# Kernel tuning notes

Measured on AMD Instinct MI355X. Metric: run time of the kernel, lower is better.

The kernel has to match this reference:

```python
import jax, jax.numpy as jnp
import numpy as np

B, T, TB, TV, TR = 4, 512, 512, 512, 256
D, H = 1024, 16
HD = D // H
D4 = D // 4
DFF = 4096
ROPE_THETA = 10000.0


def _rms(x, w, eps=1e-6):
    return x * jax.lax.rsqrt(jnp.mean(x * x, -1, keepdims=True) + eps) * w


def _ln(x, w, b, eps=1e-5):
    m = jnp.mean(x, -1, keepdims=True)
    v = jnp.var(x, -1, keepdims=True)
    return (x - m) * jax.lax.rsqrt(v + eps) * w + b


def _rope_cs(L, hd):
    inv = 1.0 / (ROPE_THETA ** (jnp.arange(0, hd, 2, dtype=jnp.float32) / hd))
    f = jnp.arange(L, dtype=jnp.float32)[:, None] * inv[None, :]
    e = jnp.concatenate([f, f], -1)  # (L, hd)
    return jnp.cos(e), jnp.sin(e)


def _rot_half(x):
    h = x.shape[-1] // 2
    return jnp.concatenate([-x[..., h:], x[..., :h]], -1)


def _rope(x, cos, sin):
    return x * cos + _rot_half(x) * sin


def _heads(x):
    b, l, _ = x.shape
    return x.reshape(b, l, H, HD).transpose(0, 2, 1, 3)  # (B,H,L,hd)


def setup_inputs() -> dict:
    key = jax.random.key(0)
    ks = jax.random.split(key, 16)
    def n(k, shape, s=0.02):
        return jax.random.normal(k, shape, jnp.float32) * s
    return {
        'x': n(ks[0], (B, T, D), 1.0),
        'bev_tokens': n(ks[1], (B, TB, D), 1.0),
        'vl_tokens': n(ks[2], (B, TV, D), 1.0),
        'reasoning_tokens': n(ks[3], (B, TR, D), 1.0),
        'conditioning': n(ks[4], (B, D), 1.0),
        'ln_pre_w': jnp.ones((D,)), 'ln_pre_b': jnp.zeros((D,)),
        'adaln_w': n(ks[5], (6 * D, D)), 'adaln_b': jnp.zeros((6 * D,)),
        'q_proj_w': n(ks[6], (D, D)), 'q_proj_b': jnp.zeros((D,)),
        'qa_w': n(ks[7], (3, D4, D)), 'qa_b': jnp.zeros((3, D4)),
        'qa_out_w': n(ks[8], (D, D4)), 'qa_out_b': jnp.zeros((D,)),
        'k_w': n(ks[9], (4, D, D)), 'k_b': jnp.zeros((4, D)),
        'v_w': n(ks[10], (4, D, D)), 'v_b': jnp.zeros((4, D)),
        'o_w': n(ks[11], (D, D)), 'o_b': jnp.zeros((D,)),
        'qn_w': jnp.ones((HD,)), 'kn_w': jnp.ones((HD,)),
        'gating': jnp.full((1,), 0.5, jnp.float32),
        'temps': jnp.zeros((4,)), 'score_biases': jnp.zeros((4,)),
        'ffn_ln_w': jnp.ones((D,)), 'ffn_ln_b': jnp.zeros((D,)),
        'ffn_w1': n(ks[12], (DFF, D)), 'ffn_b1': jnp.zeros((DFF,)),
        'ffn_w2': n(ks[13], (D, DFF)), 'ffn_b2': jnp.zeros((D,)),
    }


def reference(x, bev_tokens, vl_tokens, reasoning_tokens, conditioning,
              ln_pre_w, ln_pre_b, adaln_w, adaln_b,
              q_proj_w, q_proj_b, qa_w, qa_b, qa_out_w, qa_out_b,
              k_w, k_b, v_w, v_b, o_w, o_b, qn_w, kn_w,
              gating, temps, score_biases,
              ffn_ln_w, ffn_ln_b, ffn_w1, ffn_b1, ffn_w2, ffn_b2):
    # AdaLN modulation (T_route == 0 path: single modulation for whole sequence)
    mod = jax.nn.silu(conditioning) @ adaln_w.T + adaln_b  # (B, 6D)
    shift_pre, scale_pre, gate_attn, shift_ffn, scale_ffn, gate_ffn = jnp.split(mod, 6, axis=1)
    x_norm = _ln(x, ln_pre_w, ln_pre_b) * (1.0 + scale_pre[:, None, :]) + shift_pre[:, None, :]

    # Self Q and per-source K/V (sources: self, bev, vl, reasoning)
    q_self = _heads(x_norm @ q_proj_w.T + q_proj_b)
    srcs = [x_norm, bev_tokens, vl_tokens, reasoning_tokens]
    k_all = [_heads(s @ k_w[i].T + k_b[i]) for i, s in enumerate(srcs)]
    v_all = [_heads(s @ v_w[i].T + v_b[i]) for i, s in enumerate(srcs)]

    # Source-specific adapter queries: d -> d/4 -> d (shared out proj)
    q_ad = [_heads((x_norm @ qa_w[i].T + qa_b[i]) @ qa_out_w.T + qa_out_b) for i in range(3)]

    # QK-Norm (RMSNorm on head_dim)
    q_all = [_rms(q, qn_w) for q in [q_self] + q_ad]
    k_all = [_rms(k, kn_w) for k in k_all]

    # RoPE: Q and K for self-attention; K only for cross sources
    cosT, sinT = _rope_cs(x.shape[1], HD)
    q_all[0] = _rope(q_all[0], cosT, sinT)
    k_roped = []
    for k in k_all:
        c, s = _rope_cs(k.shape[2], HD)
        k_roped.append(_rope(k, c, s))

    # Per-source temperature / bias; gating only on reasoning scores
    temp = 1.0 + jax.nn.softplus(temps)
    ratio_g = jnp.tanh(gating[0])
    inv_sqrt_d = HD ** -0.5
    scores = []
    for i in range(4):
        s = jnp.einsum('bhqd,bhkd->bhqk', q_all[i], k_roped[i]) * (inv_sqrt_d * temp[i]) + score_biases[i]
        if i == 3:
            s = s * ratio_g
        scores.append(s)

    attn = jax.nn.softmax(jnp.concatenate(scores, -1), axis=-1)  # joint softmax
    v_cat = jnp.concatenate(v_all, 2)  # (B,H,T+TB+TV+TR,hd)
    out = jnp.einsum('bhqk,bhkd->bhqd', attn, v_cat)
    out = out.transpose(0, 2, 1, 3).reshape(x.shape) @ o_w.T + o_b
    x = x + gate_attn[:, None, :] * out

    # FFN with AdaLN modulation (dropout = identity at eval)
    h = _ln(x, ffn_ln_w, ffn_ln_b) * (1.0 + scale_ffn[:, None, :]) + shift_ffn[:, None, :]
    h = jax.nn.gelu(h @ ffn_w1.T + ffn_b1, approximate=False) @ ffn_w2.T + ffn_b2
    return x + gate_ffn[:, None, :] * h
```

## Files before the change

### kernel.cpp

```cpp
#include <hip/hip_runtime.h>

typedef unsigned short ushort_t;
typedef __attribute__((ext_vector_type(8))) __bf16 bf16x8;
typedef __attribute__((ext_vector_type(4))) float f32x4;

__device__ __forceinline__ float bf2f(ushort_t u) {
    union { unsigned int i; float f; } v; v.i = ((unsigned int)u) << 16; return v.f;
}
__device__ __forceinline__ ushort_t f2bf(float f) {
    union { float f; unsigned int i; } v; v.f = f;
    unsigned int r = (v.i + 0x7FFFu + ((v.i >> 16) & 1u)) >> 16;
    return (ushort_t)r;
}
__device__ __forceinline__ float gelu_exact(float v) {
    return 0.5f * v * (1.f + erff(v * 0.70710678118654752f));
}
__device__ __forceinline__ float ld1(const void* p, size_t i, int isf32) {
    return isf32 ? ((const float*)p)[i] : bf2f(((const ushort_t*)p)[i]);
}
__device__ __forceinline__ void stage8(const void* p, size_t idx, int isf32, ushort_t* dst) {
    if (isf32) {
        const float* f = (const float*)p + idx;
        float4 u = *(const float4*)f;
        float4 v = *(const float4*)(f + 4);
        dst[0] = f2bf(u.x); dst[1] = f2bf(u.y); dst[2] = f2bf(u.z); dst[3] = f2bf(u.w);
        dst[4] = f2bf(v.x); dst[5] = f2bf(v.y); dst[6] = f2bf(v.z); dst[7] = f2bf(v.w);
    } else {
        *(uint4*)dst = *(const uint4*)((const ushort_t*)p + idx);
    }
}
__device__ __forceinline__ void gload16(const ushort_t* g, ushort_t* l) {
    __builtin_amdgcn_global_load_lds(
        (const __attribute__((address_space(1))) unsigned int*)g,
        (__attribute__((address_space(3))) unsigned int*)l, 16, 0, 0);
}

__device__ __forceinline__ void store_q(ushort_t* qbuf, int row, int c, int p0, float v) {
    int b = row >> 9, t = row & 511;
    qbuf[((((size_t)(b * 16 + (c >> 6))) * 4 + p0) * 512 + t) * 64 + (c & 63)] = f2bf(v);
}
__device__ __forceinline__ void store_k(ushort_t* kbuf, int row, int c, int koff, int p1, float v) {
    int b = row >> p1, t = row & ((1 << p1) - 1);
    kbuf[(((size_t)(b * 16 + (c >> 6))) * 1792 + koff + t) * 64 + (c & 63)] = f2bf(v);
}
__device__ __forceinline__ void store_v(ushort_t* vbufT, int row, int c, int koff, int p1, float v) {
    int b = row >> p1, t = row & ((1 << p1) - 1);
    vbufT[(((size_t)(b * 16 + (c >> 6))) * 64 + (c & 63)) * 1792 + koff + t] = f2bf(v);
}

__global__ void detect_kernel(const unsigned int* __restrict__ x, int* __restrict__ flag) {
    if (threadIdx.x == 0 && blockIdx.x == 0) {
        int sane = 0;
        for (int i = 0; i < 256; i++) {
            unsigned int e = (x[i] >> 7) & 0xFFu;
            if (e == 0u || (e >= 100u && e <= 140u)) sane++;
        }
        *flag = (sane >= 200) ? 0 : 1;
    }
}

__global__ void prep_rope_kernel(float* __restrict__ tab) {
    int idx = blockIdx.x * 256 + threadIdx.x;
    int t = idx >> 5, d = idx & 31;
    float ang = (float)t * __expf(-(float)d * (9.210340371976184f / 32.f));
    float cs, sn;
    sincosf(ang, &sn, &cs);
    tab[idx * 2]     = cs;
    tab[idx * 2 + 1] = sn;
}

static constexpr size_t CW_QPROJ = 0;
static constexpr size_t CW_QA    = 1048576;
static constexpr size_t CW_QAOUT = 1835008;
static constexpr size_t CW_KW    = 2097152;
static constexpr size_t CW_VW    = 6291456;
static constexpr size_t CW_OW    = 10485760;
static constexpr size_t CW_FFN1  = 11534336;
static constexpr size_t CW_FFN2  = 15728640;
static constexpr size_t CW_TOTAL = 19922944;

__global__ void __launch_bounds__(256) convert_weights_kernel(
    const void* s0, const void* s1, const void* s2, const void* s3,
    const void* s4, const void* s5, const void* s6, const void* s7,
    ushort_t* __restrict__ dst, const int* __restrict__ dflag) {
    int isf32 = *dflag;
    size_t i8 = ((size_t)blockIdx.x * 256 + threadIdx.x) * 8;
    if (i8 >= CW_TOTAL) return;
    const void* src; size_t base;
    if      (i8 < CW_QA)    { src = s0; base = CW_QPROJ; }
    else if (i8 < CW_QAOUT) { src = s1; base = CW_QA; }
    else if (i8 < CW_KW)    { src = s2; base = CW_QAOUT; }
    else if (i8 < CW_VW)    { src = s3; base = CW_KW; }
    else if (i8 < CW_OW)    { src = s4; base = CW_VW; }
    else if (i8 < CW_FFN1)  { src = s5; base = CW_OW; }
    else if (i8 < CW_FFN2)  { src = s6; base = CW_FFN1; }
    else                    { src = s7; base = CW_FFN2; }
    ushort_t t8[8];
    stage8(src, i8 - base, isf32, t8);
    *(uint4*)(dst + i8) = *(uint4*)t8;
}

__global__ void __launch_bounds__(256) convert_act3_kernel(
    const void* __restrict__ bev, const void* __restrict__ vl,
    const void* __restrict__ reas, ushort_t* __restrict__ actA,
    ushort_t* __restrict__ actB, const int* __restrict__ dflag) {
    int isf32 = *dflag;
    size_t i8 = ((size_t)blockIdx.x * 256 + threadIdx.x) * 8;
    if (i8 >= 5242880) return;
    ushort_t t8[8];
    if (i8 < 2097152) {
        stage8(bev, i8, isf32, t8);
        *(uint4*)(actA + i8) = *(uint4*)t8;
    } else if (i8 < 4194304) {
        stage8(vl, i8 - 2097152, isf32, t8);
        *(uint4*)(actA + i8) = *(uint4*)t8;
    } else {
        stage8(reas, i8 - 4194304, isf32, t8);
        *(uint4*)(actB + (i8 - 4194304)) = *(uint4*)t8;
    }
}

__global__ void prep_consts_kernel(const void* __restrict__ temps,
                                   const void* __restrict__ biases,
                                   const void* __restrict__ gating,
                                   float* __restrict__ consts,
                                   const int* __restrict__ dflag) {
    if (threadIdx.x == 0 && blockIdx.x == 0) {
        int isf32 = *dflag;
        float g = tanhf(ld1(gating, 0, isf32));
        for (int s = 0; s < 4; s++) {
            float t  = ld1(temps, s, isf32);
            float sp = (t > 20.f) ? t : log1pf(expf(t));
            float scale = 0.125f * (1.f + sp);
            float mul = (s == 3) ? g : 1.f;
            consts[s]     = scale * mul;
            consts[4 + s] = ld1(biases, s, isf32) * mul;
        }
    }
}

__global__ void __launch_bounds__(256) adaln_kernel(
    const void* __restrict__ cond, const void* __restrict__ w,
    const void* __restrict__ bias, float* __restrict__ mod,
    int wmode, const int* __restrict__ dflag) {
    __shared__ float cs[1024];
    int isf32 = *dflag;
    int wf = (wmode == 2) ? 0 : isf32;
    int b = blockIdx.y, tid = threadIdx.x;
    for (int i = tid; i < 1024; i += 256) {
        float c = ld1(cond, b * 1024 + i, isf32);
        cs[i] = c / (1.f + expf(-c));
    }
    __syncthreads();
    int n = blockIdx.x * 256 + tid;
    float acc = 0.f;
    if (wf) {
        const float* wr = (const float*)w + (size_t)n * 1024;
        for (int d = 0; d < 1024; d += 8) {
            float4 a = *(const float4*)(wr + d);
            float4 bb = *(const float4*)(wr + d + 4);
            acc += cs[d+0]*a.x + cs[d+1]*a.y + cs[d+2]*a.z + cs[d+3]*a.w
                 + cs[d+4]*bb.x + cs[d+5]*bb.y + cs[d+6]*bb.z + cs[d+7]*bb.w;
        }
    } else {
        const ushort_t* wr = (const ushort_t*)w + (size_t)n * 1024;
        for (int d = 0; d < 1024; d += 8) {
            uint4 raw = *(const uint4*)(wr + d);
            const ushort_t* u = (const ushort_t*)&raw;
            acc += cs[d+0]*bf2f(u[0]) + cs[d+1]*bf2f(u[1]) + cs[d+2]*bf2f(u[2]) + cs[d+3]*bf2f(u[3])
                 + cs[d+4]*bf2f(u[4]) + cs[d+5]*bf2f(u[5]) + cs[d+6]*bf2f(u[6]) + cs[d+7]*bf2f(u[7]);
        }
    }
    mod[(size_t)b * 6144 + n] = acc + ld1(bias, n, isf32);
}

template <int SRC>
__global__ void __launch_bounds__(256) ln_mod_kernel(
    const void* __restrict__ xin, const float* __restrict__ mod,
    const void* __restrict__ lnw, const void* __restrict__ lnb,
    int shift_off, int scale_off, ushort_t* __restrict__ out,
    const int* __restrict__ dflag) {
    int isf32 = *dflag;
    int row = blockIdx.x, tid = threadIdx.x;
    int b = row >> 9;
    float v[4];
    #pragma unroll
    for (int i = 0; i < 4; i++) {
        size_t idx = (size_t)row * 1024 + tid + 256 * i;
        v[i] = (SRC == 1) ? ((const float*)xin)[idx] : ld1(xin, idx, isf32);
    }
    float s = v[0] + v[1] + v[2] + v[3];
    float ss = v[0]*v[0] + v[1]*v[1] + v[2]*v[2] + v[3]*v[3];
    #pragma unroll
    for (int off = 1; off < 64; off <<= 1) {
        s  += __shfl_xor(s,  off, 64);
        ss += __shfl_xor(ss, off, 64);
    }
    __shared__ float red[8];
    int w = tid >> 6;
    if ((tid & 63) == 0) { red[w] = s; red[4 + w] = ss; }
    __syncthreads();
    s  = red[0] + red[1] + red[2] + red[3];
    ss = red[4] + red[5] + red[6] + red[7];
    float mean = s * (1.f / 1024.f);
    float var  = ss * (1.f / 1024.f) - mean * mean;
    float inv  = rsqrtf(var + 1e-5f);
    const float* mb = mod + (size_t)b * 6144;
    #pragma unroll
    for (int i = 0; i < 4; i++) {
        int d = tid + 256 * i;
        float xn = (v[i] - mean) * inv;
        float y  = xn * ld1(lnw, d, isf32) + ld1(lnb, d, isf32);
        out[(size_t)row * 1024 + d] = f2bf(y * (1.f + mb[scale_off + d]) + mb[shift_off + d]);
    }
}

template <int EPI>
__global__ void __launch_bounds__(256) gemm_bt_kernel(
    const void* __restrict__ A, int lda,
    const void* __restrict__ W, int wrow0,
    const void* __restrict__ bias,
    void* __restrict__ Cout, int ldc, int K, int p0, int p1,
    int a_ext, int wmode, const int* __restrict__ dflag) {
    __shared__ ushort_t As[64][40];
    __shared__ ushort_t Bs[64][40];
    int isf32 = *dflag;
    int fa = a_ext ? isf32 : 0;
    int fw = (wmode == 2) ? 0 : isf32;
    int m0 = blockIdx.x * 64, n0 = blockIdx.y * 64;
    int tid = threadIdx.x;
    int r = tid >> 2, c = (tid & 3) * 8;
    int w = tid >> 6, ln = tid & 63;
    int msub = (w & 1) * 32, nsub = (w >> 1) * 32;
    int fr = ln & 15, q = ln >> 4;
    f32x4 acc00 = {0.f,0.f,0.f,0.f}, acc01 = {0.f,0.f,0.f,0.f};
    f32x4 acc10 = {0.f,0.f,0.f,0.f}, acc11 = {0.f,0.f,0.f,0.f};
    for (int k0 = 0; k0 < K; k0 += 32) {
        __syncthreads();
        {
            ushort_t t8[8];
            stage8(A, (size_t)(m0 + r) * lda + c + k0, fa, t8);
            *(uint4*)&As[r][c] = *(uint4*)t8;
        }
        {
            ushort_t t8[8];
            stage8(W, (size_t)(wrow0 + n0 + r) * K + c + k0, fw, t8);
            *(uint4*)&Bs[r][c] = *(uint4*)t8;
        }
        __syncthreads();
        bf16x8 a0 = *(const bf16x8*)&As[msub + fr][q * 8];
        bf16x8 a1 = *(const bf16x8*)&As[msub + 16 + fr][q * 8];
        bf16x8 b0 = *(const bf16x8*)&Bs[nsub + fr][q * 8];
        bf16x8 b1 = *(const bf16x8*)&Bs[nsub + 16 + fr][q * 8];
        acc00 = __builtin_amdgcn_mfma_f32_16x16x32_bf16(a0, b0, acc00, 0, 0, 0);
        acc01 = __builtin_amdgcn_mfma_f32_16x16x32_bf16(a0, b1, acc01, 0, 0, 0);
        acc10 = __builtin_amdgcn_mfma_f32_16x16x32_bf16(a1, b0, acc10, 0, 0, 0);
        acc11 = __builtin_amdgcn_mfma_f32_16x16x32_bf16(a1, b1, acc11, 0, 0, 0);
    }
    int col0 = n0 + nsub + fr;
    float bv0 = ld1(bias, wrow0 + col0, isf32);
    float bv1 = ld1(bias, wrow0 + col0 + 16, isf32);
    #pragma unroll
    for (int mi = 0; mi < 2; mi++) {
        #pragma unroll
        for (int ni = 0; ni < 2; ni++) {
            f32x4 a = (mi == 0) ? (ni == 0 ? acc00 : acc01) : (ni == 0 ? acc10 : acc11);
            int col = col0 + ni * 16;
            float bb = (ni == 0) ? bv0 : bv1;
            #pragma unroll
            for (int e = 0; e < 4; e++) {
                int rowg = m0 + msub + mi * 16 + q * 4 + e;
                float v = a[e] + bb;
                if (EPI == 2) v = gelu_exact(v);
                if (EPI == 0) {
                    ((float*)Cout)[(size_t)rowg * ldc + col] = v;
                } else if (EPI == 1 || EPI == 2) {
                    ((ushort_t*)Cout)[(size_t)rowg * ldc + col] = f2bf(v);
                } else if (EPI == 3) {
                    store_k((ushort_t*)Cout, rowg, col, p0, p1, v);
                } else if (EPI == 5) {
                    store_v((ushort_t*)Cout, rowg, col, p0, p1, v);
                } else {
                    store_q((ushort_t*)Cout, rowg, col, p0, v);
                }
            }
        }
    }
}

__device__ __forceinline__ void gemm_mainloop(
    const ushort_t* __restrict__ A, int lda,
    const ushort_t* __restrict__ W, int ldw,
    int m0, int wrow0, int kbeg, int klen,
    ushort_t* As, ushort_t* Bs, f32x4 acc[4][4])
{
    const int tid = threadIdx.x;
    const int w = tid >> 6;
    const int ln = tid & 63;
    const int fr = ln & 15, q = ln >> 4;
    const int wm = w & 1, wn = w >> 1;
    const ushort_t* gA = A + (size_t)(m0 + (tid >> 2)) * lda + kbeg + (tid & 3) * 8;
    const ushort_t* gW = W + (size_t)(wrow0 + (tid >> 2)) * ldw + kbeg + (tid & 3) * 8;
    const size_t sA = (size_t)64 * lda;
    const size_t sW = (size_t)64 * ldw;
    ushort_t* lA = As + w * 512;
    ushort_t* lB = Bs + w * 512;
    for (int k = 0; k < klen; k += 32) {
        __syncthreads();
        gload16(gA, lA);
        gload16(gA + sA, lA + 2048);
        gload16(gW, lB);
        gload16(gW + sW, lB + 2048);
        gA += 32; gW += 32;
        __syncthreads();
        bf16x8 af[4], bfr[4];
        #pragma unroll
        for (int mi = 0; mi < 4; mi++)
            af[mi] = *(const bf16x8*)&As[(wm * 64 + mi * 16 + fr) * 32 + q * 8];
        #pragma unroll
        for (int ni = 0; ni < 4; ni++)
            bfr[ni] = *(const bf16x8*)&Bs[(wn * 64 + ni * 16 + fr) * 32 + q * 8];
        #pragma unroll
        for (int mi = 0; mi < 4; mi++)
            #pragma unroll
            for (int ni = 0; ni < 4; ni++)
                acc[mi][ni] = __builtin_amdgcn_mfma_f32_16x16x32_bf16(af[mi], bfr[ni], acc[mi][ni], 0, 0, 0);
    }
}

__global__ void __launch_bounds__(256) gemm_stage1_kernel(
    const ushort_t* __restrict__ xnorm,
    const ushort_t* __restrict__ actA, const ushort_t* __restrict__ actB,
    const ushort_t* __restrict__ Wq, const ushort_t* __restrict__ Wqa,
    const ushort_t* __restrict__ Wk, const ushort_t* __restrict__ Wv,
    const void* __restrict__ bq, const void* __restrict__ bqa,
    const void* __restrict__ bk, const void* __restrict__ bv,
    const void* __restrict__ qnw, const void* __restrict__ knw,
    const float* __restrict__ ropetab,
    ushort_t* __restrict__ qbuf, ushort_t* __restrict__ qah,
    ushort_t* __restrict__ kbuf, ushort_t* __restrict__ vbufT,
    const int* __restrict__ dflag)
{
    __shared__ ushort_t As[4096], Bs[4096];
    int isf32 = *dflag;
    int bid = blockIdx.x;
    int mode, koff = 0, p1 = 9, srow0, wrow0, am0, boff = 0;
    const ushort_t* A;
    const ushort_t* W;
    const void* bias;
    if (bid < 480) {
        int bx = bid % 16, by = bid / 16;
        am0 = bx * 128; srow0 = am0;
        int n0 = by * 128;
        A = xnorm;
        if (n0 < 1024)      { mode = 0; W = Wq;  bias = bq;  wrow0 = n0; }
        else if (n0 < 1792) { mode = 1; W = Wqa; bias = bqa; wrow0 = n0 - 1024; }
        else if (n0 < 2816) { mode = 2; W = Wk;  bias = bk;  wrow0 = n0 - 1792; }
        else                { mode = 3; W = Wv;  bias = bv;  wrow0 = n0 - 2816; }
    } else {
        int id2 = bid - 480;
        int mb = id2 % 40, ny = id2 / 40;
        int src;
        if (mb < 16)      { src = 0; A = actA; am0 = mb * 128;        srow0 = am0;             koff = 512;  p1 = 9; }
        else if (mb < 32) { src = 1; A = actA; am0 = mb * 128;        srow0 = (mb - 16) * 128; koff = 1024; p1 = 9; }
        else              { src = 2; A = actB; am0 = (mb - 32) * 128; srow0 = am0;             koff = 1536; p1 = 8; }
        int n0 = ny * 128;
        int isK = (n0 < 1024);
        wrow0 = isK ? n0 : n0 - 1024;
        W = (isK ? Wk : Wv) + (size_t)(src + 1) * 1048576;
        bias = isK ? bk : bv;
        boff = (src + 1) * 1024;
        mode = isK ? 2 : 3;
    }
    f32x4 acc[4][4];
    #pragma unroll
    for (int i = 0; i < 4; i++)
        #pragma unroll
        for (int j = 0; j < 4; j++) acc[i][j] = (f32x4){0.f, 0.f, 0.f, 0.f};
    gemm_mainloop(A, 1024, W, 1024, am0, wrow0, 0, 1024, As, Bs, acc);
    int tid = threadIdx.x, w = tid >> 6, ln = tid & 63;
    int fr = ln & 15, q = tid & 63; q = (ln >> 4);
    int wm = w & 1, wn = w >> 1;
    float bb[4], nw[4];
    #pragma unroll
    for (int ni = 0; ni < 4; ni++)
        bb[ni] = ld1(bias, boff + wrow0 + wn * 64 + ni * 16 + fr, isf32);
    if (mode == 0 || mode == 2) {
        const void* nwp = (mode == 0) ? qnw : knw;
        #pragma unroll
        for (int ni = 0; ni < 4; ni++) nw[ni] = ld1(nwp, ni * 16 + fr, isf32);
    }
    const int tmask = (1 << p1) - 1;
    #pragma unroll
    for (int mi = 0; mi < 4; mi++) {
        #pragma unroll
        for (int e = 0; e < 4; e++) {
            int row = srow0 + wm * 64 + mi * 16 + q * 4 + e;
            float v0 = acc[mi][0][e] + bb[0];
            float v1 = acc[mi][1][e] + bb[1];
            float v2 = acc[mi][2][e] + bb[2];
            float v3 = acc[mi][3][e] + bb[3];
            int c0 = wrow0 + wn * 64 + fr;
            if (mode == 1) {
                qah[(size_t)row * 768 + c0]      = f2bf(v0);
                qah[(size_t)row * 768 + c0 + 16] = f2bf(v1);
                qah[(size_t)row * 768 + c0 + 32] = f2bf(v2);
                qah[(size_t)row * 768 + c0 + 48] = f2bf(v3);
            } else if (mode == 3) {
                store_v(vbufT, row, c0,      koff, p1, v0);
                store_v(vbufT, row, c0 + 16, koff, p1, v1);
                store_v(vbufT, row, c0 + 32, koff, p1, v2);
                store_v(vbufT, row, c0 + 48, koff, p1, v3);
            } else {
                float ss = v0*v0 + v1*v1 + v2*v2 + v3*v3;
                ss += __shfl_xor(ss, 1, 64);
                ss += __shfl_xor(ss, 2, 64);
                ss += __shfl_xor(ss, 4, 64);
                ss += __shfl_xor(ss, 8, 64);
                float inv = rsqrtf(ss * (1.f / 64.f) + 1e-6f);
                float y0 = v0 * inv * nw[0];
                float y1 = v1 * inv * nw[1];
                float y2 = v2 * inv * nw[2];
                float y3 = v3 * inv * nw[3];
                int t = row & tmask;
                float2 cs0 = *(const float2*)&ropetab[((t << 5) + fr) * 2];
                float2 cs1 = *(const float2*)&ropetab[((t << 5) + 16 + fr) * 2];
                float r0 = y0 * cs0.x - y2 * cs0.y;
                float r1 = y1 * cs1.x - y3 * cs1.y;
                float r2 = y2 * cs0.x + y0 * cs0.y;
                float r3 = y3 * cs1.x + y1 * cs1.y;
                if (mode == 0) {
                    store_q(qbuf, row, c0,      0, r0);
                    store_q(qbuf, row, c0 + 16, 0, r1);
                    store_q(qbuf, row, c0 + 32, 0, r2);
                    store_q(qbuf, row, c0 + 48, 0, r3);
                } else {
                    store_k(kbuf, row, c0,      koff, p1, r0);
                    store_k(kbuf, row, c0 + 16, koff, p1, r1);
                    store_k(kbuf, row, c0 + 32, koff, p1, r2);
                    store_k(kbuf, row, c0 + 48, koff, p1, r3);
                }
            }
        }
    }
}

__global__ void __launch_bounds__(256) gemm_qaout_kernel(
    const ushort_t* __restrict__ qah,
    const ushort_t* __restrict__ W, const void* __restrict__ bias,
    const void* __restrict__ qnw,
    ushort_t* __restrict__ qbuf, const int* __restrict__ dflag)
{
    __shared__ ushort_t As[4096], Bs[4096];
    int isf32 = *dflag;
    int m0 = blockIdx.x * 128, n0 = blockIdx.y * 128;
    int z = blockIdx.z;
    const ushort_t* A = qah + (size_t)z * 256;
    f32x4 acc[4][4];
    #pragma unroll
    for (int i = 0; i < 4; i++)
        #pragma unroll
        for (int j = 0; j < 4; j++) acc[i][j] = (f32x4){0.f, 0.f, 0.f, 0.f};
    gemm_mainloop(A, 768, W, 256, m0, n0, 0, 256, As, Bs, acc);
    int tid = threadIdx.x, w = tid >> 6, ln = tid & 63;
    int fr = ln & 15, q = ln >> 4, wm = w & 1, wn = w >> 1;
    float bb[4], nw[4];
    #pragma unroll
    for (int ni = 0; ni < 4; ni++) {
        bb[ni] = ld1(bias, n0 + wn * 64 + ni * 16 + fr, isf32);
        nw[ni] = ld1(qnw, ni * 16 + fr, isf32);
    }
    #pragma unroll
    for (int mi = 0; mi < 4; mi++) {
        #pragma unroll
        for (int e = 0; e < 4; e++) {
            int row = m0 + wm * 64 + mi * 16 + q * 4 + e;
            float v0 = acc[mi][0][e] + bb[0];
            float v1 = acc[mi][1][e] + bb[1];
            float v2 = acc[mi][2][e] + bb[2];
            float v3 = acc[mi][3][e] + bb[3];
            float ss = v0*v0 + v1*v1 + v2*v2 + v3*v3;
            ss += __shfl_xor(ss, 1, 64);
            ss += __shfl_xor(ss, 2, 64);
            ss += __shfl_xor(ss, 4, 64);
            ss += __shfl_xor(ss, 8, 64);
            float inv = rsqrtf(ss * (1.f / 64.f) + 1e-6f);
            int c0 = n0 + wn * 64 + fr;
            store_q(qbuf, row, c0,      1 + z, v0 * inv * nw[0]);
            store_q(qbuf, row, c0 + 16, 1 + z, v1 * inv * nw[1]);
            store_q(qbuf, row, c0 + 32, 1 + z, v2 * inv * nw[2]);
            store_q(qbuf, row, c0 + 48, 1 + z, v3 * inv * nw[3]);
        }
    }
}

template <int EPI>
__global__ void __launch_bounds__(256) gemm_plain_kernel(
    const ushort_t* __restrict__ A, int lda,
    const ushort_t* __restrict__ W, int ldw,
    const void* __restrict__ bias,
    void* __restrict__ o0, void* __restrict__ o1,
    void* __restrict__ o2, void* __restrict__ o3,
    int ldc, int ksub, const int* __restrict__ dflag)
{
    __shared__ ushort_t As[4096], Bs[4096];
    int isf32 = *dflag;
    int m0 = blockIdx.x * 128, n0 = blockIdx.y * 128;
    int z = blockIdx.z;
    void* Cout = (z == 0) ? o0 : (z == 1) ? o1 : (z == 2) ? o2 : o3;
    f32x4 acc[4][4];
    #pragma unroll
    for (int i = 0; i < 4; i++)
        #pragma unroll
        for (int j = 0; j < 4; j++) acc[i][j] = (f32x4){0.f, 0.f, 0.f, 0.f};
    gemm_mainloop(A, lda, W, ldw, m0, n0, z * ksub, ksub, As, Bs, acc);
    int tid = threadIdx.x, w = tid >> 6, ln = tid & 63;
    int fr = ln & 15, q = ln >> 4, wm = w & 1, wn = w >> 1;
    #pragma unroll
    for (int ni = 0; ni < 4; ni++) {
        int c = n0 + wn * 64 + ni * 16 + fr;
        float bb = (z == 0) ? ld1(bias, c, isf32) : 0.f;
        #pragma unroll
        for (int mi = 0; mi < 4; mi++) {
            #pragma unroll
            for (int e = 0; e < 4; e++) {
                int row = m0 + wm * 64 + mi * 16 + q * 4 + e;
                float v = acc[mi][ni][e] + bb;
                if (EPI == 2) {
                    ((ushort_t*)Cout)[(size_t)row * ldc + c] = f2bf(gelu_exact(v));
                } else {
                    ((float*)Cout)[(size_t)row * ldc + c] = v;
                }
            }
        }
    }
}

__global__ void __launch_bounds__(256) qrope_ip_kernel(
    ushort_t* __restrict__ qbuf, const void* __restrict__ qnw,
    const int* __restrict__ dflag) {
    int isf32 = *dflag;
    int w = threadIdx.x >> 6, ln = threadIdx.x & 63;
    int flat = blockIdx.x * 4 + w;
    int t = flat & 511, s = (flat >> 9) & 3;
    ushort_t* p = qbuf + (size_t)flat * 64;
    float x = bf2f(p[ln]);
    float ssum = x * x;
    #pragma unroll
    for (int off = 1; off < 64; off <<= 1) ssum += __shfl_xor(ssum, off, 64);
    float y = x * rsqrtf(ssum * (1.f / 64.f) + 1e-6f) * ld1(qnw, ln, isf32);
    if (s == 0) {
        float ang = (float)t * __expf(-(float)(ln & 31) * (9.210340371976184f / 32.f));
        float cs, sn;
        sincosf(ang, &sn, &cs);
        float other = __shfl_xor(y, 32, 64);
        y = y * cs + ((ln < 32) ? -other : other) * sn;
    }
    p[ln] = f2bf(y);
}

__global__ void __launch_bounds__(256) krope_ip_kernel(
    ushort_t* __restrict__ kbuf, const void* __restrict__ knw,
    const int* __restrict__ dflag) {
    int isf32 = *dflag;
    int w = threadIdx.x >> 6, ln = threadIdx.x & 63;
    int flat = blockIdx.x * 4 + w;
    int j = flat % 1792;
    int t = j & 511;
    ushort_t* p = kbuf + (size_t)flat * 64;
    float x = bf2f(p[ln]);
    float ssum = x * x;
    #pragma unroll
    for (int off = 1; off < 64; off <<= 1) ssum += __shfl_xor(ssum, off, 64);
    float y = x * rsqrtf(ssum * (1.f / 64.f) + 1e-6f) * ld1(knw, ln, isf32);
    float ang = (float)t * __expf(-(float)(ln & 31) * (9.210340371976184f / 32.f));
    float cs, sn;
    sincosf(ang, &sn, &cs);
    float other = __shfl_xor(y, 32, 64);
    y = y * cs + ((ln < 32) ? -other : other) * sn;
    p[ln] = f2bf(y);
}

__global__ void __launch_bounds__(256) attn_mfma_kernel(
    const ushort_t* __restrict__ qbuf, const ushort_t* __restrict__ kbuf,
    const ushort_t* __restrict__ vbufT, const float* __restrict__ consts,
    float* __restrict__ pacc0, float* __restrict__ pacc1,
    float* __restrict__ pml) {
    __shared__ ushort_t ks[64][72];
    __shared__ ushort_t vsT[64][72];
    __shared__ ushort_t ps[4][16][72];
    int id = blockIdx.x;
    int g  = (id & 7) | ((id >> 6) << 3);
    int qx = (id >> 3) & 7;
    int bh = g & 63;
    int z  = g >> 6;
    int tid = threadIdx.x, w = tid >> 6, ln = tid & 63;
    int r0 = qx * 64 + w * 16;
    int m = ln & 15, quad = ln >> 4;
    const int ntile = z ? 12 : 16;
    const int keybase = z * 1024;
    const int s0i = z * 2;

    const ushort_t* qb = qbuf + (size_t)bh * 4 * 512 * 64;
    bf16x8 qA0f = *(const bf16x8*)(qb + ((size_t)(s0i * 512 + r0 + m)) * 64 + quad * 8);
    bf16x8 qA1f = *(const bf16x8*)(qb + ((size_t)(s0i * 512 + r0 + m)) * 64 + 32 + quad * 8);
    bf16x8 qB0f = *(const bf16x8*)(qb + ((size_t)((s0i + 1) * 512 + r0 + m)) * 64 + quad * 8);
    bf16x8 qB1f = *(const bf16x8*)(qb + ((size_t)((s0i + 1) * 512 + r0 + m)) * 64 + 32 + quad * 8);

    const float aA = consts[s0i],     bA = consts[4 + s0i];
    const float aB = consts[s0i + 1], bB = consts[4 + s0i + 1];

    float m_i[4], l_i[4];
    f32x4 acc[4];
    #pragma unroll
    for (int e = 0; e < 4; e++) { m_i[e] = -1e30f; l_i[e] = 0.f; }
    #pragma unroll
    for (int d = 0; d < 4; d++) acc[d] = (f32x4){0.f, 0.f, 0.f, 0.f};

    const ushort_t* kb  = kbuf  + (size_t)bh * 1792 * 64 + (size_t)keybase * 64;
    const ushort_t* vbT = vbufT + (size_t)bh * 64 * 1792 + keybase;
    int skey = tid >> 3, sd = (tid & 7) * 8;
    uint4 kreg0 = *(const uint4*)(kb + (size_t)skey * 64 + sd);
    uint4 kreg1 = *(const uint4*)(kb + (size_t)(skey + 32) * 64 + sd);
    uint4 vreg0 = *(const uint4*)(vbT + (size_t)skey * 1792 + sd);
    uint4 vreg1 = *(const uint4*)(vbT + (size_t)(skey + 32) * 1792 + sd);
    *(uint4*)&ks[skey][sd]       = kreg0;
    *(uint4*)&ks[skey + 32][sd]  = kreg1;
    *(uint4*)&vsT[skey][sd]      = vreg0;
    *(uint4*)&vsT[skey + 32][sd] = vreg1;
    __syncthreads();

    for (int ti = 0; ti < ntile; ti++) {
        const bool pf = (ti + 1 < ntile);
        if (pf) {
            int nx = (ti + 1) * 64;
            kreg0 = *(const uint4*)(kb + (size_t)(nx + skey) * 64 + sd);
            kreg1 = *(const uint4*)(kb + (size_t)(nx + skey + 32) * 64 + sd);
            vreg0 = *(const uint4*)(vbT + (size_t)skey * 1792 + nx + sd);
            vreg1 = *(const uint4*)(vbT + (size_t)(skey + 32) * 1792 + nx + sd);
        }
        int sl = (ti >= 8) ? 1 : 0;
        float a_s = sl ? aB : aA;
        float b_s = sl ? bB : bA;
        bf16x8 qA0 = sl ? qB0f : qA0f;
        bf16x8 qA1 = sl ? qB1f : qA1f;
        f32x4 zero = {0.f, 0.f, 0.f, 0.f};
        bf16x8 k0a = *(const bf16x8*)&ks[m][quad * 8];
        bf16x8 k0b = *(const bf16x8*)&ks[m][32 + quad * 8];
        bf16x8 k1a = *(const bf16x8*)&ks[16 + m][quad * 8];
        bf16x8 k1b = *(const bf16x8*)&ks[16 + m][32 + quad * 8];
        bf16x8 k2a = *(const bf16x8*)&ks[32 + m][quad * 8];
        bf16x8 k2b = *(const bf16x8*)&ks[32 + m][32 + quad * 8];
        bf16x8 k3a = *(const bf16x8*)&ks[48 + m][quad * 8];
        bf16x8 k3b = *(const bf16x8*)&ks[48 + m][32 + quad * 8];
        f32x4 sc0 = __builtin_amdgcn_mfma_f32_16x16x32_bf16(qA0, k0a, zero, 0, 0, 0);
        sc0 = __builtin_amdgcn_mfma_f32_16x16x32_bf16(qA1, k0b, sc0, 0, 0, 0);
        f32x4 sc1 = __builtin_amdgcn_mfma_f32_16x16x32_bf16(qA0, k1a, zero, 0, 0, 0);
        sc1 = __builtin_amdgcn_mfma_f32_16x16x32_bf16(qA1, k1b, sc1, 0, 0, 0);
// ... 183 lines not shown
            bf16x8 pA0 = *(const bf16x8*)&ps[w][m][quad * 8];
            bf16x8 pA1 = *(const bf16x8*)&ps[w][m][32 + quad * 8];
            #pragma unroll
            for (int dsub = 0; dsub < 4; dsub++) {
                bf16x8 vB0 = *(const bf16x8*)&vsT[p][dsub * 16 + m][quad * 8];
                bf16x8 vB1 = *(const bf16x8*)&vsT[p][dsub * 16 + m][32 + quad * 8];
                acc[dsub] = __builtin_amdgcn_mfma_f32_16x16x32_bf16(pA0, vB0, acc[dsub], 0, 0, 0);
                acc[dsub] = __builtin_amdgcn_mfma_f32_16x16x32_bf16(pA1, vB1, acc[dsub], 0, 0, 0);
            }
            if (tcnt < 27) {
                *(uint4*)&ks[1 - p][skey][sd]       = kreg0;
                *(uint4*)&ks[1 - p][skey + 32][sd]  = kreg1;
                *(uint4*)&vsT[1 - p][skey][sd]      = vreg0;
                *(uint4*)&vsT[1 - p][skey + 32][sd] = vreg1;
            }
            __syncthreads();
            p ^= 1;
            tcnt++;
        }
    }
    #pragma unroll
    for (int e = 0; e < 4; e++) {
        float l = l_i[e];
        #pragma unroll
        for (int off = 1; off < 16; off <<= 1) l += __shfl_xor(l, off, 64);
        float invl = 1.f / l;
        int t = r0 + quad * 4 + e;
        #pragma unroll
        for (int dsub = 0; dsub < 4; dsub++) {
            int d = dsub * 16 + m;
            attn_out[(((size_t)(b * 512 + t)) * 16 + h) * 64 + d] = f2bf(acc[dsub][e] * invl);
        }
    }
}

__global__ void resgate_kernel(const void* __restrict__ x, const float* __restrict__ p0,
                               const float* __restrict__ p1, const float* __restrict__ p2,
                               const float* __restrict__ p3,
                               const float* __restrict__ mod, float* __restrict__ x1,
                               int sum4, const int* __restrict__ dflag) {
    int isf32 = *dflag;
    int i = blockIdx.x * 256 + threadIdx.x;
    int b = i >> 19, n = i & 1023;
    float proj = p0[i];
    if (sum4) proj += p1[i] + p2[i] + p3[i];
    x1[i] = ld1(x, i, isf32) + mod[(size_t)b * 6144 + 2048 + n] * proj;
}
__global__ void final_kernel(const float* __restrict__ x1, const float* __restrict__ f0,
                             const float* __restrict__ f1, const float* __restrict__ f2,
                             const float* __restrict__ f3,
                             const float* __restrict__ mod, void* __restrict__ out,
                             int sum4, const int* __restrict__ dflag) {
    int isf32 = *dflag;
    int i = blockIdx.x * 256 + threadIdx.x;
    int b = i >> 19, n = i & 1023;
    float ffn = f0[i];
    if (sum4) ffn += f1[i] + f2[i] + f3[i];
    float val = x1[i] + mod[(size_t)b * 6144 + 5120 + n] * ffn;
    if (isf32) ((float*)out)[i] = val;
    else       ((ushort_t*)out)[i] = f2bf(val);
}

static constexpr size_t OFF_CONSTS   = 0;
static constexpr size_t OFF_FLAG     = 64;
static constexpr size_t OFF_MOD      = 512;
static constexpr size_t OFF_XNORM    = OFF_MOD    + 98304;
static constexpr size_t OFF_QAH      = OFF_XNORM  + 4194304;
static constexpr size_t OFF_KBUF     = OFF_XNORM  + 8388608;
static constexpr size_t OFF_VBUF     = OFF_KBUF   + 14680064;
static constexpr size_t OFF_QBUF     = OFF_VBUF   + 14680064;
static constexpr size_t OFF_ATTNOUT  = OFF_QBUF   + 16777216;
static constexpr size_t OFF_WCACHE   = OFF_ATTNOUT + 4194304;
static constexpr size_t OFF_PACC1    = OFF_WCACHE + CW_TOTAL * 2;
static constexpr size_t OFF_PML      = OFF_PACC1  + 8388608;
static constexpr size_t OFF_ROPE     = OFF_PML    + 524288;
static constexpr size_t WS_NEED      = OFF_WCACHE + 52428800;

extern "C" void kernel_launch(void* const* d_in, const int* in_sizes, int n_in,
                              void* d_out, int out_size, void* d_ws, size_t ws_size,
                              hipStream_t stream) {
    (void)in_sizes; (void)n_in; (void)out_size;
    const void* x        = d_in[0];
    const void* bev      = d_in[1];
    const void* vl       = d_in[2];
    const void* reas     = d_in[3];
    const void* cond     = d_in[4];
    const void* ln_pre_w = d_in[5];
    const void* ln_pre_b = d_in[6];
    const void* adaln_w  = d_in[7];
    const void* adaln_b  = d_in[8];
    const void* q_proj_w = d_in[9];
    const void* q_proj_b = d_in[10];
    const void* qa_w     = d_in[11];
    const void* qa_b     = d_in[12];
    const void* qa_out_w = d_in[13];
    const void* qa_out_b = d_in[14];
    const void* k_w      = d_in[15];
    const void* k_b      = d_in[16];
    const void* v_w      = d_in[17];
    const void* v_b      = d_in[18];
    const void* o_w      = d_in[19];
    const void* o_b      = d_in[20];
    const void* qn_w     = d_in[21];
    const void* kn_w     = d_in[22];
    const void* gating   = d_in[23];
    const void* temps    = d_in[24];
    const void* sbias    = d_in[25];
    const void* ffn_ln_w = d_in[26];
    const void* ffn_ln_b = d_in[27];
    const void* ffn_w1   = d_in[28];
    const void* ffn_b1   = d_in[29];
    const void* ffn_w2   = d_in[30];
    const void* ffn_b2   = d_in[31];

    char* ws = (char*)d_ws;
    float*    consts   = (float*)(ws + OFF_CONSTS);
    int*      dflag    = (int*)(ws + OFF_FLAG);
    float*    mod      = (float*)(ws + OFF_MOD);
    ushort_t* xnorm    = (ushort_t*)(ws + OFF_XNORM);
    ushort_t* qah      = (ushort_t*)(ws + OFF_QAH);
    ushort_t* kbuf     = (ushort_t*)(ws + OFF_KBUF);
    ushort_t* vbufT    = (ushort_t*)(ws + OFF_VBUF);
    ushort_t* qbuf     = (ushort_t*)(ws + OFF_QBUF);
    ushort_t* attnout  = (ushort_t*)(ws + OFF_ATTNOUT);
    float*    x1       = (float*)(ws + OFF_XNORM);
    ushort_t* hmid     = (ushort_t*)(ws + OFF_KBUF);
    ushort_t* hin      = (ushort_t*)(ws + OFF_ATTNOUT);
    ushort_t* wc       = (ushort_t*)(ws + OFF_WCACHE);
    float*    ropetab  = (float*)(ws + OFF_ROPE);
    float*    pacc0    = (float*)(ws + OFF_XNORM);
    float*    pacc1    = (float*)(ws + OFF_PACC1);
    float*    pml      = (float*)(ws + OFF_PML);
    ushort_t* actA     = (ushort_t*)(ws + OFF_PACC1);
    ushort_t* actB     = (ushort_t*)(ws + OFF_ATTNOUT);
    float*    op0      = (float*)(ws + OFF_KBUF);
    float*    op1      = (float*)(ws + OFF_KBUF + 8388608);
    float*    op2      = (float*)(ws + OFF_KBUF + 16777216);
    float*    op3      = (float*)(ws + OFF_QBUF);
    float*    f0       = (float*)(ws + OFF_QBUF);
    float*    f1       = (float*)(ws + OFF_QBUF + 8388608);
    float*    f2       = (float*)(ws + OFF_KBUF + 16777216);
    float*    f3       = (float*)(ws + OFF_PACC1);

    const bool use_cache = (ws_size >= WS_NEED);

    detect_kernel<<<1, 64, 0, stream>>>((const unsigned int*)x, dflag);
    prep_consts_kernel<<<1, 64, 0, stream>>>(temps, sbias, gating, consts, dflag);

    if (use_cache) {
        prep_rope_kernel<<<64, 256, 0, stream>>>(ropetab);
        convert_weights_kernel<<<9728, 256, 0, stream>>>(
            q_proj_w, qa_w, qa_out_w, k_w, v_w, o_w, ffn_w1, ffn_w2, wc, dflag);
        convert_act3_kernel<<<2560, 256, 0, stream>>>(bev, vl, reas, actA, actB, dflag);
        adaln_kernel<<<dim3(24, 4), 256, 0, stream>>>(cond, adaln_w, adaln_b, mod, 0, dflag);
        ln_mod_kernel<0><<<2048, 256, 0, stream>>>(x, mod, ln_pre_w, ln_pre_b, 0, 1024, xnorm, dflag);

        gemm_stage1_kernel<<<1120, 256, 0, stream>>>(
            xnorm, actA, actB,
            wc + CW_QPROJ, wc + CW_QA, wc + CW_KW, wc + CW_VW,
            q_proj_b, qa_b, k_b, v_b, qn_w, kn_w, ropetab,
            qbuf, qah, kbuf, vbufT, dflag);
        gemm_qaout_kernel<<<dim3(16, 8, 3), 256, 0, stream>>>(
            qah, wc + CW_QAOUT, qa_out_b, qn_w, qbuf, dflag);

        attn_mfma_kernel<<<1024, 256, 0, stream>>>(
            qbuf, kbuf, vbufT, consts, pacc0, pacc1, pml);
        attn_combine_kernel<<<8192, 256, 0, stream>>>(pacc0, pacc1, pml, attnout);

        gemm_plain_kernel<0><<<dim3(16, 8, 4), 256, 0, stream>>>(
            attnout, 1024, wc + CW_OW, 1024, o_b, op0, op1, op2, op3, 1024, 256, dflag);
        resgate_kernel<<<8192, 256, 0, stream>>>(x, op0, op1, op2, op3, mod, x1, 1, dflag);
        ln_mod_kernel<1><<<2048, 256, 0, stream>>>(x1, mod, ffn_ln_w, ffn_ln_b, 3072, 4096, hin, dflag);
        gemm_plain_kernel<2><<<dim3(16, 32, 1), 256, 0, stream>>>(
            hin, 1024, wc + CW_FFN1, 1024, ffn_b1, hmid, nullptr, nullptr, nullptr, 4096, 1024, dflag);
        gemm_plain_kernel<0><<<dim3(16, 8, 4), 256, 0, stream>>>(
            hmid, 4096, wc + CW_FFN2, 4096, ffn_b2, f0, f1, f2, f3, 1024, 1024, dflag);
        final_kernel<<<8192, 256, 0, stream>>>(x1, f0, f1, f2, f3, mod, d_out, 1, dflag);
    } else {
        float* proj0L = (float*)(ws + OFF_QBUF);
        adaln_kernel<<<dim3(24, 4), 256, 0, stream>>>(cond, adaln_w, adaln_b, mod, 0, dflag);
        ln_mod_kernel<0><<<2048, 256, 0, stream>>>(x, mod, ln_pre_w, ln_pre_b, 0, 1024, xnorm, dflag);
        gemm_bt_kernel<4><<<dim3(32, 16), 256, 0, stream>>>(xnorm, 1024, q_proj_w, 0, q_proj_b, qbuf, 0, 1024, 0, 9, 0, 0, dflag);
        {
            const void* srcs[4] = {xnorm, bev, vl, reas};
            const int koffs[4] = {0, 512, 1024, 1536};
            const int p1s[4]   = {9, 9, 9, 8};
            for (int i = 0; i < 4; i++) {
                int aext = (i == 0) ? 0 : 1;
                int gx = (i == 3) ? 16 : 32;
                gemm_bt_kernel<3><<<dim3(gx, 16), 256, 0, stream>>>(
                    srcs[i], 1024, k_w, i * 1024, k_b, kbuf, 0, 1024, koffs[i], p1s[i], aext, 0, dflag);
                gemm_bt_kernel<5><<<dim3(gx, 16), 256, 0, stream>>>(
                    srcs[i], 1024, v_w, i * 1024, v_b, vbufT, 0, 1024, koffs[i], p1s[i], aext, 0, dflag);
            }
        }
        gemm_bt_kernel<1><<<dim3(32, 12), 256, 0, stream>>>(xnorm, 1024, qa_w, 0, qa_b, qah, 768, 1024, 0, 0, 0, 0, dflag);
        for (int i = 0; i < 3; i++)
            gemm_bt_kernel<4><<<dim3(32, 16), 256, 0, stream>>>(qah + i * 256, 768, qa_out_w, 0, qa_out_b,
                                                                qbuf, 0, 256, 1 + i, 9, 0, 0, dflag);
        qrope_ip_kernel<<<32768, 256, 0, stream>>>(qbuf, qn_w, dflag);
        krope_ip_kernel<<<28672, 256, 0, stream>>>(kbuf, kn_w, dflag);
        attn_mfma_legacy_kernel<<<dim3(8, 64), 256, 0, stream>>>(qbuf, kbuf, vbufT, consts, attnout);
        gemm_bt_kernel<0><<<dim3(32, 16), 256, 0, stream>>>(attnout, 1024, o_w, 0, o_b, proj0L, 1024, 1024, 0, 0, 0, 0, dflag);
        resgate_kernel<<<8192, 256, 0, stream>>>(x, proj0L, proj0L, proj0L, proj0L, mod, x1, 0, dflag);
        ln_mod_kernel<1><<<2048, 256, 0, stream>>>(x1, mod, ffn_ln_w, ffn_ln_b, 3072, 4096, hin, dflag);
        gemm_bt_kernel<2><<<dim3(32, 64), 256, 0, stream>>>(hin, 1024, ffn_w1, 0, ffn_b1, hmid, 4096, 1024, 0, 0, 0, 0, dflag);
        gemm_bt_kernel<0><<<dim3(32, 16), 256, 0, stream>>>(hmid, 4096, ffn_w2, 0, ffn_b2, proj0L, 1024, 4096, 0, 0, 0, 0, dflag);
        final_kernel<<<8192, 256, 0, stream>>>(x1, proj0L, proj0L, proj0L, proj0L, mod, d_out, 0, dflag);
    }
}
```

Measured before the change: 526.3 us.

## Double GEMM K-step, split AdaLN over K with atomics, fuse resgate with LN

```diff
diff --git a/kernel.cpp b/kernel.cpp
--- a/kernel.cpp
+++ b/kernel.cpp
@@ -139,39 +139,46 @@
     }
 }
 
+__global__ void adaln_init_kernel(const void* __restrict__ bias, float* __restrict__ mod,
+                                  const int* __restrict__ dflag) {
+    int isf32 = *dflag;
+    int n = blockIdx.x * 256 + threadIdx.x;
+    float b = ld1(bias, n, isf32);
+    #pragma unroll
+    for (int bb = 0; bb < 4; bb++) mod[(size_t)bb * 6144 + n] = b;
+}
+
 __global__ void __launch_bounds__(256) adaln_kernel(
     const void* __restrict__ cond, const void* __restrict__ w,
-    const void* __restrict__ bias, float* __restrict__ mod,
-    int wmode, const int* __restrict__ dflag) {
-    __shared__ float cs[1024];
-    int isf32 = *dflag;
-    int wf = (wmode == 2) ? 0 : isf32;
-    int b = blockIdx.y, tid = threadIdx.x;
-    for (int i = tid; i < 1024; i += 256) {
-        float c = ld1(cond, b * 1024 + i, isf32);
-        cs[i] = c / (1.f + expf(-c));
+    float* __restrict__ mod, const int* __restrict__ dflag) {
+    __shared__ float cs[256];
+    int isf32 = *dflag;
+    int b = blockIdx.y, z = blockIdx.z, tid = threadIdx.x;
+    {
+        float c = ld1(cond, b * 1024 + z * 256 + tid, isf32);
+        cs[tid] = c / (1.f + expf(-c));
     }
     __syncthreads();
     int n = blockIdx.x * 256 + tid;
     float acc = 0.f;
-    if (wf) {
-        const float* wr = (const float*)w + (size_t)n * 1024;
-        for (int d = 0; d < 1024; d += 8) {
+    if (isf32) {
+        const float* wr = (const float*)w + (size_t)n * 1024 + z * 256;
+        for (int d = 0; d < 256; d += 8) {
             float4 a = *(const float4*)(wr + d);
             float4 bb = *(const float4*)(wr + d + 4);
             acc += cs[d+0]*a.x + cs[d+1]*a.y + cs[d+2]*a.z + cs[d+3]*a.w
                  + cs[d+4]*bb.x + cs[d+5]*bb.y + cs[d+6]*bb.z + cs[d+7]*bb.w;
         }
     } else {
-        const ushort_t* wr = (const ushort_t*)w + (size_t)n * 1024;
-        for (int d = 0; d < 1024; d += 8) {
+        const ushort_t* wr = (const ushort_t*)w + (size_t)n * 1024 + z * 256;
+        for (int d = 0; d < 256; d += 8) {
             uint4 raw = *(const uint4*)(wr + d);
             const ushort_t* u = (const ushort_t*)&raw;
             acc += cs[d+0]*bf2f(u[0]) + cs[d+1]*bf2f(u[1]) + cs[d+2]*bf2f(u[2]) + cs[d+3]*bf2f(u[3])
                  + cs[d+4]*bf2f(u[4]) + cs[d+5]*bf2f(u[5]) + cs[d+6]*bf2f(u[6]) + cs[d+7]*bf2f(u[7]);
         }
     }
-    mod[(size_t)b * 6144 + n] = acc + ld1(bias, n, isf32);
+    atomicAdd(&mod[(size_t)b * 6144 + n], acc);
 }
 
 template <int SRC>
@@ -212,6 +219,51 @@
         float xn = (v[i] - mean) * inv;
         float y  = xn * ld1(lnw, d, isf32) + ld1(lnb, d, isf32);
         out[(size_t)row * 1024 + d] = f2bf(y * (1.f + mb[scale_off + d]) + mb[shift_off + d]);
+    }
+}
+
+__global__ void __launch_bounds__(256) resgate_ln_kernel(
+    const void* __restrict__ x, const float* __restrict__ p0,
+    const float* __restrict__ p1, const float* __restrict__ p2,
+    const float* __restrict__ p3, const float* __restrict__ mod,
+    const void* __restrict__ lnw, const void* __restrict__ lnb,
+    float* __restrict__ x1, ushort_t* __restrict__ hin,
+    const int* __restrict__ dflag) {
+    int isf32 = *dflag;
+    int row = blockIdx.x, tid = threadIdx.x;
+    int b = row >> 9;
+    const float* mb = mod + (size_t)b * 6144;
+    float v[4];
+    #pragma unroll
+    for (int i = 0; i < 4; i++) {
+        size_t idx = (size_t)row * 1024 + tid + 256 * i;
+        int n = tid + 256 * i;
+        float proj = p0[idx] + p1[idx] + p2[idx] + p3[idx];
+        v[i] = ld1(x, idx, isf32) + mb[2048 + n] * proj;
+        x1[idx] = v[i];
+    }
+    float s = v[0] + v[1] + v[2] + v[3];
+    float ss = v[0]*v[0] + v[1]*v[1] + v[2]*v[2] + v[3]*v[3];
+    #pragma unroll
+    for (int off = 1; off < 64; off <<= 1) {
+        s  += __shfl_xor(s,  off, 64);
+        ss += __shfl_xor(ss, off, 64);
+    }
+    __shared__ float red[8];
+    int w = tid >> 6;
+    if ((tid & 63) == 0) { red[w] = s; red[4 + w] = ss; }
+    __syncthreads();
+    s  = red[0] + red[1] + red[2] + red[3];
+    ss = red[4] + red[5] + red[6] + red[7];
+    float mean = s * (1.f / 1024.f);
+    float var  = ss * (1.f / 1024.f) - mean * mean;
+    float inv  = rsqrtf(var + 1e-5f);
+    #pragma unroll
+    for (int i = 0; i < 4; i++) {
+        int d = tid + 256 * i;
+        float xn = (v[i] - mean) * inv;
+        float y  = xn * ld1(lnw, d, isf32) + ld1(lnb, d, isf32);
+        hin[(size_t)row * 1024 + d] = f2bf(y * (1.f + mb[4096 + d]) + mb[3072 + d]);
     }
 }
 
@@ -305,26 +357,33 @@
     const size_t sW = (size_t)64 * ldw;
     ushort_t* lA = As + w * 512;
     ushort_t* lB = Bs + w * 512;
-    for (int k = 0; k < klen; k += 32) {
+    for (int k = 0; k < klen; k += 64) {
         __syncthreads();
         gload16(gA, lA);
         gload16(gA + sA, lA + 2048);
+        gload16(gA + 32, lA + 4096);
+        gload16(gA + sA + 32, lA + 6144);
         gload16(gW, lB);
         gload16(gW + sW, lB + 2048);
-        gA += 32; gW += 32;
+        gload16(gW + 32, lB + 4096);
+        gload16(gW + sW + 32, lB + 6144);
+        gA += 64; gW += 64;
         __syncthreads();
-        bf16x8 af[4], bfr[4];
-        #pragma unroll
-        for (int mi = 0; mi < 4; mi++)
-            af[mi] = *(const bf16x8*)&As[(wm * 64 + mi * 16 + fr) * 32 + q * 8];
-        #pragma unroll
-        for (int ni = 0; ni < 4; ni++)
-            bfr[ni] = *(const bf16x8*)&Bs[(wn * 64 + ni * 16 + fr) * 32 + q * 8];
-        #pragma unroll
-        for (int mi = 0; mi < 4; mi++)
+        #pragma unroll
+        for (int kk = 0; kk < 2; kk++) {
+            bf16x8 af[4], bfr[4];
+            #pragma unroll
+            for (int mi = 0; mi < 4; mi++)
+                af[mi] = *(const bf16x8*)&As[kk * 4096 + (wm * 64 + mi * 16 + fr) * 32 + q * 8];
             #pragma unroll
             for (int ni = 0; ni < 4; ni++)
-                acc[mi][ni] = __builtin_amdgcn_mfma_f32_16x16x32_bf16(af[mi], bfr[ni], acc[mi][ni], 0, 0, 0);
+                bfr[ni] = *(const bf16x8*)&Bs[kk * 4096 + (wn * 64 + ni * 16 + fr) * 32 + q * 8];
+            #pragma unroll
+            for (int mi = 0; mi < 4; mi++)
+                #pragma unroll
+                for (int ni = 0; ni < 4; ni++)
+                    acc[mi][ni] = __builtin_amdgcn_mfma_f32_16x16x32_bf16(af[mi], bfr[ni], acc[mi][ni], 0, 0, 0);
+        }
     }
 }
 
@@ -341,7 +400,7 @@
     ushort_t* __restrict__ kbuf, ushort_t* __restrict__ vbufT,
     const int* __restrict__ dflag)
 {
-    __shared__ ushort_t As[4096], Bs[4096];
+    __shared__ ushort_t As[8192], Bs[8192];
     int isf32 = *dflag;
     int bid = blockIdx.x;
     int mode, koff = 0, p1 = 9, srow0, wrow0, am0, boff = 0;
@@ -379,7 +438,7 @@
         for (int j = 0; j < 4; j++) acc[i][j] = (f32x4){0.f, 0.f, 0.f, 0.f};
     gemm_mainloop(A, 1024, W, 1024, am0, wrow0, 0, 1024, As, Bs, acc);
     int tid = threadIdx.x, w = tid >> 6, ln = tid & 63;
-    int fr = ln & 15, q = tid & 63; q = (ln >> 4);
+    int fr = ln & 15, q = ln >> 4;
     int wm = w & 1, wn = w >> 1;
     float bb[4], nw[4];
     #pragma unroll
@@ -451,7 +510,7 @@
     const void* __restrict__ qnw,
     ushort_t* __restrict__ qbuf, const int* __restrict__ dflag)
 {
-    __shared__ ushort_t As[4096], Bs[4096];
+    __shared__ ushort_t As[8192], Bs[8192];
     int isf32 = *dflag;
     int m0 = blockIdx.x * 128, n0 = blockIdx.y * 128;
     int z = blockIdx.z;
@@ -503,7 +562,7 @@
     void* __restrict__ o2, void* __restrict__ o3,
     int ldc, int ksub, const int* __restrict__ dflag)
 {
-    __shared__ ushort_t As[4096], Bs[4096];
+    __shared__ ushort_t As[8192], Bs[8192];
     int isf32 = *dflag;
     int m0 = blockIdx.x * 128, n0 = blockIdx.y * 128;
     int z = blockIdx.z;
@@ -993,7 +1052,8 @@
         convert_weights_kernel<<<9728, 256, 0, stream>>>(
             q_proj_w, qa_w, qa_out_w, k_w, v_w, o_w, ffn_w1, ffn_w2, wc, dflag);
         convert_act3_kernel<<<2560, 256, 0, stream>>>(bev, vl, reas, actA, actB, dflag);
-        adaln_kernel<<<dim3(24, 4), 256, 0, stream>>>(cond, adaln_w, adaln_b, mod, 0, dflag);
+        adaln_init_kernel<<<24, 256, 0, stream>>>(adaln_b, mod, dflag);
+        adaln_kernel<<<dim3(24, 4, 4), 256, 0, stream>>>(cond, adaln_w, mod, dflag);
         ln_mod_kernel<0><<<2048, 256, 0, stream>>>(x, mod, ln_pre_w, ln_pre_b, 0, 1024, xnorm, dflag);
 
         gemm_stage1_kernel<<<1120, 256, 0, stream>>>(
@@ -1010,8 +1070,8 @@
 
         gemm_plain_kernel<0><<<dim3(16, 8, 4), 256, 0, stream>>>(
             attnout, 1024, wc + CW_OW, 1024, o_b, op0, op1, op2, op3, 1024, 256, dflag);
-        resgate_kernel<<<8192, 256, 0, stream>>>(x, op0, op1, op2, op3, mod, x1, 1, dflag);
-        ln_mod_kernel<1><<<2048, 256, 0, stream>>>(x1, mod, ffn_ln_w, ffn_ln_b, 3072, 4096, hin, dflag);
+        resgate_ln_kernel<<<2048, 256, 0, stream>>>(
+            x, op0, op1, op2, op3, mod, ffn_ln_w, ffn_ln_b, x1, hin, dflag);
         gemm_plain_kernel<2><<<dim3(16, 32, 1), 256, 0, stream>>>(
             hin, 1024, wc + CW_FFN1, 1024, ffn_b1, hmid, nullptr, nullptr, nullptr, 4096, 1024, dflag);
         gemm_plain_kernel<0><<<dim3(16, 8, 4), 256, 0, stream>>>(
@@ -1019,7 +1079,8 @@
         final_kernel<<<8192, 256, 0, stream>>>(x1, f0, f1, f2, f3, mod, d_out, 1, dflag);
     } else {
         float* proj0L = (float*)(ws + OFF_QBUF);
-        adaln_kernel<<<dim3(24, 4), 256, 0, stream>>>(cond, adaln_w, adaln_b, mod, 0, dflag);
+        adaln_init_kernel<<<24, 256, 0, stream>>>(adaln_b, mod, dflag);
+        adaln_kernel<<<dim3(24, 4, 4), 256, 0, stream>>>(cond, adaln_w, mod, dflag);
         ln_mod_kernel<0><<<2048, 256, 0, stream>>>(x, mod, ln_pre_w, ln_pre_b, 0, 1024, xnorm, dflag);
         gemm_bt_kernel<4><<<dim3(32, 16), 256, 0, stream>>>(xnorm, 1024, q_proj_w, 0, q_proj_b, qbuf, 0, 1024, 0, 9, 0, 0, dflag);
         {
```

New measurement: 511.7 us. 2.8% less time.
